# Performance work log

Measured on AMD Instinct MI355X. Metric: run time of the kernel, lower is better.

Reference implementation:

```python
import jax, jax.numpy as jnp
import numpy as np

N_NODES = 100000
N_EDGES = 3200000
N_GRAPHS = 256
HID = 128


def _glorot(key, shape):
    fan_in = shape[1]
    return jax.random.normal(key, shape, dtype=jnp.float32) / jnp.sqrt(jnp.float32(fan_in))


def setup_inputs() -> dict:
    key = jax.random.key(0)
    ks = jax.random.split(key, 16)
    x = jax.random.normal(ks[0], (N_NODES, 50), dtype=jnp.float32)
    edge_index = jax.random.randint(ks[1], (2, N_EDGES), 0, N_NODES, dtype=jnp.int32)
    batch = jnp.sort(jax.random.randint(ks[2], (N_NODES,), 0, N_GRAPHS, dtype=jnp.int32))
    d1, d2, d3 = HID, HID * 2, HID * 4
    params = {
        'w1l': _glorot(ks[3], (d1, 50)), 'b1': jnp.zeros((d1,), jnp.float32), 'w1r': _glorot(ks[4], (d1, 50)),
        'w2l': _glorot(ks[5], (d2, d1)), 'b2': jnp.zeros((d2,), jnp.float32), 'w2r': _glorot(ks[6], (d2, d1)),
        'w3l': _glorot(ks[7], (d3, d2)), 'b3': jnp.zeros((d3,), jnp.float32), 'w3r': _glorot(ks[8], (d3, d2)),
        'fc1_w': _glorot(ks[9], (d2, d3)), 'fc1_b': jnp.zeros((d2,), jnp.float32),
        'fc2_w': _glorot(ks[10], (d1, d2)), 'fc2_b': jnp.zeros((d1,), jnp.float32),
        'cls_w': _glorot(ks[11], (15, d1)), 'cls_b': jnp.zeros((15,), jnp.float32),
    }
    return {'x': x, 'edge_index': edge_index, 'batch': batch, **params}


def _sage_conv(x, src, dst, wl, b, wr):
    # PyG SAGEConv (mean aggr): out = lin_l(mean_j x_j) + lin_r(x_i)
    agg = jax.ops.segment_sum(x[src], dst, num_segments=N_NODES)
    deg = jax.ops.segment_sum(jnp.ones((src.shape[0],), x.dtype), dst, num_segments=N_NODES)
    agg = agg / jnp.maximum(deg, 1.0)[:, None]
    return agg @ wl.T + b + x @ wr.T


def reference(x, edge_index, batch,
              w1l, b1, w1r, w2l, b2, w2r, w3l, b3, w3r,
              fc1_w, fc1_b, fc2_w, fc2_b, cls_w, cls_b):
    src, dst = edge_index[0], edge_index[1]
    # eval mode: dropout is identity
    h = jax.nn.leaky_relu(_sage_conv(x, src, dst, w1l, b1, w1r), negative_slope=0.01)
    h = jax.nn.relu(_sage_conv(h, src, dst, w2l, b2, w2r))
    h = jax.nn.relu(_sage_conv(h, src, dst, w3l, b3, w3r))
    # global mean pool over graphs
    pooled = jax.ops.segment_sum(h, batch, num_segments=N_GRAPHS)
    cnt = jax.ops.segment_sum(jnp.ones((h.shape[0],), h.dtype), batch, num_segments=N_GRAPHS)
    pooled = pooled / jnp.maximum(cnt, 1.0)[:, None]
    z = jax.nn.relu(pooled @ fc1_w.T + fc1_b)
    z = jax.nn.relu(z @ fc2_w.T + fc2_b)
    return z @ cls_w.T + cls_b
```

## Files before the change

kernel.cpp:

```cpp
#include <hip/hip_runtime.h>
#include <hip/hip_bf16.h>

#define N_NODES 100000
#define N_EDGES 3200000
#define N_GRAPHS 256
#define CAP 80
#define NB 1563
#define NPB 64
#define PBLK 512
#define EPB 6250

typedef __hip_bfloat16 bf16;
using f32x4  = __attribute__((ext_vector_type(4))) float;
using f32x2  = __attribute__((ext_vector_type(2))) float;
using short8 = __attribute__((ext_vector_type(8))) short;

__global__ __launch_bounds__(256) void p1_count(const int* __restrict__ dst,
                                                int* __restrict__ bcount) {
    __shared__ int hist[NB];
    int i = blockIdx.x;
    for (int b = threadIdx.x; b < NB; b += 256) hist[b] = 0;
    __syncthreads();
    int base = i * EPB;
    for (int j = threadIdx.x; j < EPB; j += 256)
        atomicAdd(&hist[dst[base + j] >> 6], 1);
    __syncthreads();
    for (int b = threadIdx.x; b < NB; b += 256) bcount[(size_t)b * PBLK + i] = hist[b];
}

__global__ __launch_bounds__(512) void p2a_total(const int* __restrict__ bcount,
                                                 int* __restrict__ btotal) {
    __shared__ int red[512];
    int b = blockIdx.x;
    red[threadIdx.x] = bcount[(size_t)b * PBLK + threadIdx.x];
    __syncthreads();
    for (int off = 256; off > 0; off >>= 1) {
        if (threadIdx.x < off) red[threadIdx.x] += red[threadIdx.x + off];
        __syncthreads();
    }
    if (threadIdx.x == 0) btotal[b] = red[0];
}

__global__ __launch_bounds__(1024) void p2b_scan(const int* __restrict__ btotal,
                                                 int* __restrict__ bbase) {
    __shared__ int buf[1024];
    __shared__ int carry;
    if (threadIdx.x == 0) carry = 0;
    __syncthreads();
    for (int t = 0; t < NB; t += 1024) {
        int i = t + threadIdx.x;
        int v = (i < NB) ? btotal[i] : 0;
        buf[threadIdx.x] = v;
        __syncthreads();
        for (int off = 1; off < 1024; off <<= 1) {
            int tv = (threadIdx.x >= off) ? buf[threadIdx.x - off] : 0;
            __syncthreads();
            buf[threadIdx.x] += tv;
            __syncthreads();
        }
        if (i < NB) bbase[i] = carry + buf[threadIdx.x] - v;
        __syncthreads();
        if (threadIdx.x == 0) carry += buf[1023];
        __syncthreads();
    }
    if (threadIdx.x == 0) bbase[NB] = carry;
}

__global__ __launch_bounds__(512) void p2c_off(const int* __restrict__ bcount,
                                               const int* __restrict__ bbase,
                                               int* __restrict__ off) {
    __shared__ int buf[512];
    int b = blockIdx.x;
    int v = bcount[(size_t)b * PBLK + threadIdx.x];
    buf[threadIdx.x] = v;
    __syncthreads();
    for (int o = 1; o < 512; o <<= 1) {
        int t = (threadIdx.x >= o) ? buf[threadIdx.x - o] : 0;
        __syncthreads();
        buf[threadIdx.x] += t;
        __syncthreads();
    }
    off[(size_t)threadIdx.x * NB + b] = bbase[b] + buf[threadIdx.x] - v;
}

__global__ __launch_bounds__(256) void p3_scatter(const int* __restrict__ src,
                                                  const int* __restrict__ dst,
                                                  const int* __restrict__ off,
                                                  unsigned int* __restrict__ ebuf) {
    __shared__ int loff[NB];
    int i = blockIdx.x;
    for (int b = threadIdx.x; b < NB; b += 256) loff[b] = off[(size_t)i * NB + b];
    __syncthreads();
    int base = i * EPB;
    for (int j = threadIdx.x; j < EPB; j += 256) {
        int d = dst[base + j];
        int p = atomicAdd(&loff[d >> 6], 1);
        ebuf[p] = ((unsigned)src[base + j] << 6) | (unsigned)(d & 63);
    }
}

__global__ __launch_bounds__(256) void p4_csr(const unsigned int* __restrict__ ebuf,
                                              const int* __restrict__ bbase,
                                              int* __restrict__ cols, int* __restrict__ cnt,
                                              float* __restrict__ invdeg) {
    __shared__ int lcnt[NPB];
    int b = blockIdx.x;
    if (threadIdx.x < NPB) lcnt[threadIdx.x] = 0;
    __syncthreads();
    int s = bbase[b], e = bbase[b + 1];
    int n0 = b * NPB;
    for (int j = s + threadIdx.x; j < e; j += 256) {
        unsigned int p = ebuf[j];
        int dl = p & 63;
        int r = atomicAdd(&lcnt[dl], 1);
        if (r < CAP) cols[(size_t)(n0 + dl) * CAP + r] = (int)(p >> 6);
    }
    __syncthreads();
    if (threadIdx.x < NPB) {
        int n = n0 + threadIdx.x;
        if (n < N_NODES) {
            int c = lcnt[threadIdx.x];
            cnt[n] = c;
            invdeg[n] = 1.0f / fmaxf((float)c, 1.0f);
        }
    }
}

__global__ void xprep_kernel(const float* __restrict__ x, bf16* __restrict__ xb,
                             unsigned char* __restrict__ xb8) {
    int t = blockIdx.x * blockDim.x + threadIdx.x;
    if (t >= N_NODES * 64) return;
    int n = t >> 6, f = t & 63;
    float v = (f < 50) ? x[(size_t)n * 50 + f] : 0.f;
    xb[t] = __float2bfloat16(v);
    int p = __builtin_amdgcn_cvt_pk_fp8_f32(v, v, 0, false);
    xb8[t] = (unsigned char)(p & 0xff);
}

__device__ __forceinline__ void wcvt(const float* __restrict__ s, bf16* __restrict__ d,
                                     int Din, int Kp, int lt) {
    int o = lt / Kp, kk = lt % Kp;
    d[lt] = __float2bfloat16(kk < Din ? s[(size_t)o * Din + kk] : 0.f);
}

__global__ void wprep_all_kernel(const float* w1l, const float* w1r,
                                 const float* w2l, const float* w2r,
                                 const float* w3l, const float* w3r,
                                 bf16* w1l_b, bf16* w1r_b, bf16* w2l_b, bf16* w2r_b,
                                 bf16* w3l_b, bf16* w3r_b) {
    int t = blockIdx.x * blockDim.x + threadIdx.x;
    if      (t < 8192)   wcvt(w1l, w1l_b, 50, 64, t);
    else if (t < 16384)  wcvt(w1r, w1r_b, 50, 64, t - 8192);
    else if (t < 49152)  wcvt(w2l, w2l_b, 128, 128, t - 16384);
    else if (t < 81920)  wcvt(w2r, w2r_b, 128, 128, t - 49152);
    else if (t < 212992) wcvt(w3l, w3l_b, 256, 256, t - 81920);
    else if (t < 344064) wcvt(w3r, w3r_b, 256, 256, t - 212992);
}

template <int D>
__global__ void aggv8_kernel(const unsigned char* __restrict__ h8,
                             const int* __restrict__ cnt,
                             const int* __restrict__ cols, const float* __restrict__ invdeg,
                             bf16* __restrict__ AG) {
    constexpr int L = D / 8;
    int n = blockIdx.x * (256 / L) + threadIdx.x / L;
    int lane = threadIdx.x % L;
    if (n >= N_NODES) return;
    const int* cp = cols + (size_t)n * CAP;
    int deg = min(cnt[n], CAP);
    float acc[8] = {};
    auto accum = [&](uint2 v) {
        f32x2 a0 = __builtin_amdgcn_cvt_pk_f32_fp8(v.x, false);
        f32x2 a1 = __builtin_amdgcn_cvt_pk_f32_fp8(v.x, true);
        f32x2 a2 = __builtin_amdgcn_cvt_pk_f32_fp8(v.y, false);
        f32x2 a3 = __builtin_amdgcn_cvt_pk_f32_fp8(v.y, true);
        acc[0] += a0[0]; acc[1] += a0[1]; acc[2] += a1[0]; acc[3] += a1[1];
        acc[4] += a2[0]; acc[5] += a2[1]; acc[6] += a3[0]; acc[7] += a3[1];
    };
    int j = 0;
    for (; j + 8 <= deg; j += 8) {
        uint2 v[8];
#pragma unroll
        for (int q = 0; q < 8; ++q)
            v[q] = *(const uint2*)&h8[(size_t)cp[j + q] * D + lane * 8];
#pragma unroll
        for (int q = 0; q < 8; ++q) accum(v[q]);
    }
    for (; j < deg; ++j) accum(*(const uint2*)&h8[(size_t)cp[j] * D + lane * 8]);
    float inv = invdeg[n];
    union { uint4 u; bf16 hb[8]; } o;
#pragma unroll
    for (int i = 0; i < 8; ++i) o.hb[i] = __float2bfloat16(acc[i] * inv);
    *(uint4*)&AG[(size_t)n * D + lane * 8] = o.u;
}

template <int ACT, int POOL, int OUT8, int NX>
__global__ __launch_bounds__(256) void glds_gemm(
        const bf16* __restrict__ A1, const bf16* __restrict__ A2, int Kh,
        const bf16* __restrict__ B1, const bf16* __restrict__ B2,
        const float* __restrict__ bias, bf16* __restrict__ out,
        unsigned char* __restrict__ out8,
        int M, int Dout,
        const int* __restrict__ batch, float* __restrict__ pooled) {
    __shared__ alignas(16) bf16 As[2][128][32];
    __shared__ alignas(16) bf16 Bs[2][128][32];
    __shared__ int sbatch[128];

    const int gid = blockIdx.x;
    const int group = gid / (8 * NX);
    const int rem = gid % (8 * NX);
    const int xcol = rem >> 3;
    const int ytile = group * 8 + (rem & 7);
    const int MBt = (M + 127) >> 7;
    if (ytile >= MBt) return;

    const int tid = threadIdx.x;
    const int n0 = ytile * 128;
    const int o0 = xcol * 128;

    if (POOL && tid < 128) {
        int n = n0 + tid;
        sbatch[tid] = (n < M) ? batch[n] : -1;
    }

    const int lane = tid & 63;
    const int w = tid >> 6;
    const int wr = w >> 1, wc = w & 1;
    const int lr = lane & 15, hi = lane >> 4;
    const int l4 = lane >> 2;
    const int kc8 = (lane & 3) * 8;

    f32x4 acc[4][4] = {};

    auto stage = [&](int buf, int k0) {
        const bf16* Ap;
        const bf16* Bp;
        int kk;
        if (k0 < Kh) { Ap = A1; Bp = B1; kk = k0; }
        else         { Ap = A2; Bp = B2; kk = k0 - Kh; }
#pragma unroll
        for (int c = 0; c < 2; ++c) {
            int rl = w * 32 + c * 16 + l4;
            size_t ga = (size_t)min(n0 + rl, M - 1) * (size_t)Kh + kk + kc8;
            __builtin_amdgcn_global_load_lds(
                (const __attribute__((address_space(1))) void*)(Ap + ga),
                (__attribute__((address_space(3))) void*)&As[buf][w * 32 + c * 16][0], 16, 0, 0);
            size_t gb = (size_t)(o0 + rl) * (size_t)Kh + kk + kc8;
            __builtin_amdgcn_global_load_lds(
                (const __attribute__((address_space(1))) void*)(Bp + gb),
                (__attribute__((address_space(3))) void*)&Bs[buf][w * 32 + c * 16][0], 16, 0, 0);
        }
    };

    const int nt = (2 * Kh) / 32;
    stage(0, 0);
    asm volatile("s_waitcnt vmcnt(0)\n\ts_barrier" ::: "memory");

    int cur = 0;
    for (int t = 0; t < nt; ++t) {
        if (t + 1 < nt) stage(cur ^ 1, (t + 1) * 32);

        short8 af[4], bfr[4];
#pragma unroll
        for (int m = 0; m < 4; ++m)
            af[m] = *(const short8*)&As[cur][wr * 64 + m * 16 + lr][hi * 8];
#pragma unroll
        for (int n = 0; n < 4; ++n)
            bfr[n] = *(const short8*)&Bs[cur][wc * 64 + n * 16 + lr][hi * 8];
#pragma unroll
        for (int m = 0; m < 4; ++m)
#pragma unroll
            for (int n = 0; n < 4; ++n)
                acc[m][n] = __builtin_amdgcn_mfma_f32_16x16x32_bf16(af[m], bfr[n], acc[m][n], 0, 0, 0);

        if (t + 1 < nt)
            asm volatile("s_waitcnt vmcnt(0)\n\ts_barrier" ::: "memory");
        cur ^= 1;
    }

    float bias_v[4];
#pragma unroll
    for (int n = 0; n < 4; ++n) bias_v[n] = bias[o0 + wc * 64 + n * 16 + lr];

    if (!POOL) {
#pragma unroll
        for (int m = 0; m < 4; ++m) {
#pragma unroll
            for (int j = 0; j < 4; ++j) {
                int row = n0 + wr * 64 + m * 16 + hi * 4 + j;
                if (row < M) {
#pragma unroll
                    for (int n = 0; n < 4; ++n) {
                        int col = o0 + wc * 64 + n * 16 + lr;
                        float s = acc[m][n][j] + bias_v[n];
                        if (ACT == 0) s = (s >= 0.f) ? s : 0.01f * s;
                        else          s = fmaxf(s, 0.f);
                        out[(size_t)row * Dout + col] = __float2bfloat16(s);
                        if (OUT8) {
                            int p = __builtin_amdgcn_cvt_pk_fp8_f32(s, s, 0, false);
                            out8[(size_t)row * Dout + col] = (unsigned char)(p & 0xff);
                        }
                    }
                }
            }
        }
    } else {
        int lastv = min(127, M - 1 - n0);
        int gmin = sbatch[0], gmax = sbatch[lastv];
        for (int g = gmin; g <= gmax; ++g) {
            float s[4] = {0.f, 0.f, 0.f, 0.f};
#pragma unroll
            for (int m = 0; m < 4; ++m) {
#pragma unroll
                for (int j = 0; j < 4; ++j) {
                    int rl = wr * 64 + m * 16 + hi * 4 + j;
                    if (sbatch[rl] == g) {
#pragma unroll
                        for (int n = 0; n < 4; ++n)
                            s[n] += fmaxf(acc[m][n][j] + bias_v[n], 0.f);
                    }
                }
            }
#pragma unroll
            for (int n = 0; n < 4; ++n) {
                float v = s[n];
                v += __shfl_xor(v, 16, 64);
                v += __shfl_xor(v, 32, 64);
                if (hi == 0)
                    atomicAdd(&pooled[(size_t)g * 512 + o0 + wc * 64 + n * 16 + lr], v);
            }
        }
    }
}

__global__ void bounds_kernel(const int* __restrict__ batch, int* __restrict__ gstart) {
    int g = blockIdx.x * blockDim.x + threadIdx.x;
    if (g > N_GRAPHS) return;
    int lo = 0, hi = N_NODES;
    while (lo < hi) {
        int mid = (lo + hi) >> 1;
        if (batch[mid] < g) lo = mid + 1;
        else hi = mid;
    }
    gstart[g] = lo;
}

__global__ void pool_finalize(float* __restrict__ pooled, const int* __restrict__ gstart) {
    int g = blockIdx.x;
    int f = threadIdx.x;
    float cnt = fmaxf((float)(gstart[g + 1] - gstart[g]), 1.0f);
    pooled[(size_t)g * 512 + f] /= cnt;
}

template <int ACT>
__global__ void mlp_kernel(const float* __restrict__ in, const float* __restrict__ w,
                           const float* __restrict__ b, float* __restrict__ out,
                           int M, int K, int O) {
    int t = blockIdx.x * blockDim.x + threadIdx.x;
    if (t >= M * O) return;
    int m = t / O, o = t % O;
    const float* ip = in + (size_t)m * K;
    const float* wp = w + (size_t)o * K;
    float s = 0.f;
    for (int k = 0; k < K; ++k) s += ip[k] * wp[k];
    s += b[o];
    if (ACT) s = fmaxf(s, 0.f);
    out[(size_t)m * O + o] = s;
}

extern "C" void kernel_launch(void* const* d_in, const int* in_sizes, int n_in,
                              void* d_out, int out_size, void* d_ws, size_t ws_size,
                              hipStream_t stream) {
    const float* x     = (const float*)d_in[0];
    const int*   ei    = (const int*)d_in[1];
    const int*   batch = (const int*)d_in[2];
    const float* w1l = (const float*)d_in[3];
    const float* b1  = (const float*)d_in[4];
    const float* w1r = (const float*)d_in[5];
    const float* w2l = (const float*)d_in[6];
    const float* b2  = (const float*)d_in[7];
    const float* w2r = (const float*)d_in[8];
    const float* w3l = (const float*)d_in[9];
    const float* b3  = (const float*)d_in[10];
    const float* w3r = (const float*)d_in[11];
    const float* fc1_w = (const float*)d_in[12];
    const float* fc1_b = (const float*)d_in[13];
    const float* fc2_w = (const float*)d_in[14];
    const float* fc2_b = (const float*)d_in[15];
    const float* cls_w = (const float*)d_in[16];
    const float* cls_b = (const float*)d_in[17];
    float* out = (float*)d_out;

    const int* src = ei;
    const int* dst = ei + N_EDGES;

    char* wsp = (char*)d_ws;
    size_t used = 0;
    auto alloc = [&](size_t bytes) {
        char* p = wsp + used;
        used += (bytes + 255) & ~(size_t)255;
        return p;
    };
    int*   cnt    = (int*)alloc((size_t)N_NODES * 4);
    int*   cols   = (int*)alloc((size_t)N_NODES * CAP * 4);
    float* invdeg = (float*)alloc((size_t)N_NODES * 4);
    int*   gstart = (int*)alloc((size_t)(N_GRAPHS + 1) * 4);
    bf16*  xb     = (bf16*)alloc((size_t)N_NODES * 64 * 2);
    char*  R      = alloc((size_t)N_NODES * 256 * 2);
    bf16*  AG     = (bf16*)R;
    bf16*  h1     = (bf16*)(R + (size_t)N_NODES * 128 * 2);
    bf16*  h2     = (bf16*)alloc((size_t)N_NODES * 256 * 2);
    unsigned char* h1_8 = (unsigned char*)alloc((size_t)N_NODES * 128);
    unsigned char* h2_8 = (unsigned char*)alloc((size_t)N_NODES * 256);
    bf16*  w1l_b  = (bf16*)alloc(128 * 64 * 2);
    bf16*  w1r_b  = (bf16*)alloc(128 * 64 * 2);
    bf16*  w2l_b  = (bf16*)alloc(256 * 128 * 2);
    bf16*  w2r_b  = (bf16*)alloc(256 * 128 * 2);
    bf16*  w3l_b  = (bf16*)alloc(512 * 256 * 2);
    bf16*  w3r_b  = (bf16*)alloc(512 * 256 * 2);
    float* pooled = (float*)alloc((size_t)N_GRAPHS * 512 * 4);
    float* z1     = (float*)alloc((size_t)N_GRAPHS * 256 * 4);
    float* z2     = (float*)alloc((size_t)N_GRAPHS * 128 * 4);

    int* bcount = (int*)h1_8;
    int* btotal = bcount + (size_t)NB * PBLK;
    int* bbase  = btotal + NB;
    int* off    = bbase + NB + 1;
    unsigned int* ebuf = (unsigned int*)h2;
    unsigned char* xb8 = (unsigned char*)h2;

    if (ws_size < used) return;

    p1_count<<<PBLK, 256, 0, stream>>>(dst, bcount);
    p2a_total<<<NB, 512, 0, stream>>>(bcount, btotal);
    p2b_scan<<<1, 1024, 0, stream>>>(btotal, bbase);
    p2c_off<<<NB, 512, 0, stream>>>(bcount, bbase, off);
    p3_scatter<<<PBLK, 256, 0, stream>>>(src, dst, off, ebuf);
    p4_csr<<<NB, 256, 0, stream>>>(ebuf, bbase, cols, cnt, invdeg);
    bounds_kernel<<<2, 160, 0, stream>>>(batch, gstart);

    xprep_kernel<<<(N_NODES * 64 + 255) / 256, 256, 0, stream>>>(x, xb, xb8);
    wprep_all_kernel<<<(344064 + 255) / 256, 256, 0, stream>>>(
        w1l, w1r, w2l, w2r, w3l, w3r, w1l_b, w1r_b, w2l_b, w2r_b, w3l_b, w3r_b);

    const int GB = 98 * 8;

    aggv8_kernel<64><<<(N_NODES * 8 + 255) / 256, 256, 0, stream>>>(
        xb8, cnt, cols, invdeg, AG);
    glds_gemm<0, 0, 1, 1><<<GB, 256, 0, stream>>>(
        AG, xb, 64, w1l_b, w1r_b, b1, h1, h1_8, N_NODES, 128, nullptr, nullptr);

    aggv8_kernel<128><<<(N_NODES * 16 + 255) / 256, 256, 0, stream>>>(
        h1_8, cnt, cols, invdeg, AG);
    glds_gemm<1, 0, 1, 2><<<GB * 2, 256, 0, stream>>>(
        AG, h1, 128, w2l_b, w2r_b, b2, h2, h2_8, N_NODES, 256, nullptr, nullptr);

    aggv8_kernel<256><<<(N_NODES * 32 + 255) / 256, 256, 0, stream>>>(
        h2_8, cnt, cols, invdeg, AG);
    hipMemsetAsync(pooled, 0, (size_t)N_GRAPHS * 512 * 4, stream);
    glds_gemm<1, 1, 0, 4><<<GB * 4, 256, 0, stream>>>(
        AG, h2, 256, w3l_b, w3r_b, b3, nullptr, nullptr, N_NODES, 512, batch, pooled);
    pool_finalize<<<N_GRAPHS, 512, 0, stream>>>(pooled, gstart);

    mlp_kernel<1><<<(N_GRAPHS * 256 + 255) / 256, 256, 0, stream>>>(
        pooled, fc1_w, fc1_b, z1, N_GRAPHS, 512, 256);
    mlp_kernel<1><<<(N_GRAPHS * 128 + 255) / 256, 256, 0, stream>>>(
        z1, fc2_w, fc2_b, z2, N_GRAPHS, 256, 128);
    mlp_kernel<0><<<(N_GRAPHS * 15 + 255) / 256, 256, 0, stream>>>(
        z2, cls_w, cls_b, out, N_GRAPHS, 128, 15);
}
```

Before: 585.4 us.

## Store GEMM A operands and aggregates in fp8, convert to bf16 in-kernel

The aggregation kernel now writes its mean-aggregated features as fp8 instead of bf16, and the layer GEMMs read both A halves (aggregate and self features) from fp8 buffers. The fp8 bytes are converted to bf16 in registers before being written to shared memory, replacing the direct global-to-LDS loads for A. Layer outputs are written only in fp8, and the bf16 copies of x and the hidden layers are no longer produced. This roughly halves A-side and output memory traffic. The cost is extra conversion ALU work, a register-staged A path, and lower precision in the root and aggregate terms.

```diff
diff --git a/kernel.cpp b/kernel.cpp
--- a/kernel.cpp
+++ b/kernel.cpp
@@ -126,13 +126,11 @@
     }
 }
 
-__global__ void xprep_kernel(const float* __restrict__ x, bf16* __restrict__ xb,
-                             unsigned char* __restrict__ xb8) {
+__global__ void xprep_kernel(const float* __restrict__ x, unsigned char* __restrict__ xb8) {
     int t = blockIdx.x * blockDim.x + threadIdx.x;
     if (t >= N_NODES * 64) return;
     int n = t >> 6, f = t & 63;
     float v = (f < 50) ? x[(size_t)n * 50 + f] : 0.f;
-    xb[t] = __float2bfloat16(v);
     int p = __builtin_amdgcn_cvt_pk_fp8_f32(v, v, 0, false);
     xb8[t] = (unsigned char)(p & 0xff);
 }
@@ -161,7 +159,7 @@
 __global__ void aggv8_kernel(const unsigned char* __restrict__ h8,
                              const int* __restrict__ cnt,
                              const int* __restrict__ cols, const float* __restrict__ invdeg,
-                             bf16* __restrict__ AG) {
+                             unsigned char* __restrict__ AG8) {
     constexpr int L = D / 8;
     int n = blockIdx.x * (256 / L) + threadIdx.x / L;
     int lane = threadIdx.x % L;
@@ -188,18 +186,33 @@
     }
     for (; j < deg; ++j) accum(*(const uint2*)&h8[(size_t)cp[j] * D + lane * 8]);
     float inv = invdeg[n];
-    union { uint4 u; bf16 hb[8]; } o;
-#pragma unroll
-    for (int i = 0; i < 8; ++i) o.hb[i] = __float2bfloat16(acc[i] * inv);
-    *(uint4*)&AG[(size_t)n * D + lane * 8] = o.u;
-}
-
-template <int ACT, int POOL, int OUT8, int NX>
-__global__ __launch_bounds__(256) void glds_gemm(
-        const bf16* __restrict__ A1, const bf16* __restrict__ A2, int Kh,
+    uint2 o;
+    int w0 = __builtin_amdgcn_cvt_pk_fp8_f32(acc[0] * inv, acc[1] * inv, 0, false);
+    w0     = __builtin_amdgcn_cvt_pk_fp8_f32(acc[2] * inv, acc[3] * inv, w0, true);
+    int w1 = __builtin_amdgcn_cvt_pk_fp8_f32(acc[4] * inv, acc[5] * inv, 0, false);
+    w1     = __builtin_amdgcn_cvt_pk_fp8_f32(acc[6] * inv, acc[7] * inv, w1, true);
+    o.x = (unsigned)w0; o.y = (unsigned)w1;
+    *(uint2*)&AG8[(size_t)n * D + lane * 8] = o;
+}
+
+__device__ __forceinline__ short8 cvt8(uint2 v) {
+    f32x2 p0 = __builtin_amdgcn_cvt_pk_f32_fp8(v.x, false);
+    f32x2 p1 = __builtin_amdgcn_cvt_pk_f32_fp8(v.x, true);
+    f32x2 p2 = __builtin_amdgcn_cvt_pk_f32_fp8(v.y, false);
+    f32x2 p3 = __builtin_amdgcn_cvt_pk_f32_fp8(v.y, true);
+    union { short8 s; bf16 h[8]; } r;
+    r.h[0] = __float2bfloat16(p0[0]); r.h[1] = __float2bfloat16(p0[1]);
+    r.h[2] = __float2bfloat16(p1[0]); r.h[3] = __float2bfloat16(p1[1]);
+    r.h[4] = __float2bfloat16(p2[0]); r.h[5] = __float2bfloat16(p2[1]);
+    r.h[6] = __float2bfloat16(p3[0]); r.h[7] = __float2bfloat16(p3[1]);
+    return r.s;
+}
+
+template <int ACT, int POOL, int NX>
+__global__ __launch_bounds__(256) void fp8a_gemm(
+        const unsigned char* __restrict__ A1, const unsigned char* __restrict__ A2, int Kh,
         const bf16* __restrict__ B1, const bf16* __restrict__ B2,
-        const float* __restrict__ bias, bf16* __restrict__ out,
-        unsigned char* __restrict__ out8,
+        const float* __restrict__ bias, unsigned char* __restrict__ out8,
         int M, int Dout,
         const int* __restrict__ batch, float* __restrict__ pooled) {
     __shared__ alignas(16) bf16 As[2][128][32];
@@ -232,33 +245,46 @@
 
     f32x4 acc[4][4] = {};
 
-    auto stage = [&](int buf, int k0) {
-        const bf16* Ap;
-        const bf16* Bp;
-        int kk;
-        if (k0 < Kh) { Ap = A1; Bp = B1; kk = k0; }
-        else         { Ap = A2; Bp = B2; kk = k0 - Kh; }
+    const int rl0 = w * 32 + l4;
+    const int rl1 = rl0 + 16;
+
+    auto issueA = [&](int k0, uint2& a0, uint2& a1v) {
+        const unsigned char* Ap = (k0 < Kh) ? A1 : A2;
+        int kk = (k0 < Kh) ? k0 : k0 - Kh;
+        a0  = *(const uint2*)&Ap[(size_t)min(n0 + rl0, M - 1) * Kh + kk + kc8];
+        a1v = *(const uint2*)&Ap[(size_t)min(n0 + rl1, M - 1) * Kh + kk + kc8];
+    };
+    auto issueB = [&](int buf, int k0) {
+        const bf16* Bp = (k0 < Kh) ? B1 : B2;
+        int kk = (k0 < Kh) ? k0 : k0 - Kh;
 #pragma unroll
         for (int c = 0; c < 2; ++c) {
             int rl = w * 32 + c * 16 + l4;
-            size_t ga = (size_t)min(n0 + rl, M - 1) * (size_t)Kh + kk + kc8;
-            __builtin_amdgcn_global_load_lds(
-                (const __attribute__((address_space(1))) void*)(Ap + ga),
-                (__attribute__((address_space(3))) void*)&As[buf][w * 32 + c * 16][0], 16, 0, 0);
             size_t gb = (size_t)(o0 + rl) * (size_t)Kh + kk + kc8;
             __builtin_amdgcn_global_load_lds(
                 (const __attribute__((address_space(1))) void*)(Bp + gb),
                 (__attribute__((address_space(3))) void*)&Bs[buf][w * 32 + c * 16][0], 16, 0, 0);
         }
     };
+    auto writeA = [&](int buf, uint2 a0, uint2 a1v) {
+        *(short8*)&As[buf][rl0][kc8] = cvt8(a0);
+        *(short8*)&As[buf][rl1][kc8] = cvt8(a1v);
+    };
 
     const int nt = (2 * Kh) / 32;
-    stage(0, 0);
-    asm volatile("s_waitcnt vmcnt(0)\n\ts_barrier" ::: "memory");
+    uint2 ra0, ra1;
+    issueA(0, ra0, ra1);
+    issueB(0, 0);
+    asm volatile("s_waitcnt vmcnt(0)" ::: "memory");
+    writeA(0, ra0, ra1);
+    __syncthreads();
 
     int cur = 0;
     for (int t = 0; t < nt; ++t) {
-        if (t + 1 < nt) stage(cur ^ 1, (t + 1) * 32);
+        if (t + 1 < nt) {
+            issueA((t + 1) * 32, ra0, ra1);
+            issueB(cur ^ 1, (t + 1) * 32);
+        }
 
         short8 af[4], bfr[4];
 #pragma unroll
@@ -273,8 +299,11 @@
             for (int n = 0; n < 4; ++n)
                 acc[m][n] = __builtin_amdgcn_mfma_f32_16x16x32_bf16(af[m], bfr[n], acc[m][n], 0, 0, 0);
 
-        if (t + 1 < nt)
-            asm volatile("s_waitcnt vmcnt(0)\n\ts_barrier" ::: "memory");
+        if (t + 1 < nt) {
+            asm volatile("s_waitcnt vmcnt(0)" ::: "memory");
+            writeA(cur ^ 1, ra0, ra1);
+            __syncthreads();
+        }
         cur ^= 1;
     }
 
@@ -295,11 +324,8 @@
                         float s = acc[m][n][j] + bias_v[n];
                         if (ACT == 0) s = (s >= 0.f) ? s : 0.01f * s;
                         else          s = fmaxf(s, 0.f);
-                        out[(size_t)row * Dout + col] = __float2bfloat16(s);
-                        if (OUT8) {
-                            int p = __builtin_amdgcn_cvt_pk_fp8_f32(s, s, 0, false);
-                            out8[(size_t)row * Dout + col] = (unsigned char)(p & 0xff);
-                        }
+                        int p = __builtin_amdgcn_cvt_pk_fp8_f32(s, s, 0, false);
+                        out8[(size_t)row * Dout + col] = (unsigned char)(p & 0xff);
                     }
                 }
             }
@@ -405,11 +431,10 @@
     int*   cols   = (int*)alloc((size_t)N_NODES * CAP * 4);
     float* invdeg = (float*)alloc((size_t)N_NODES * 4);
     int*   gstart = (int*)alloc((size_t)(N_GRAPHS + 1) * 4);
-    bf16*  xb     = (bf16*)alloc((size_t)N_NODES * 64 * 2);
+    char*  xbdead = alloc((size_t)N_NODES * 64 * 2);
     char*  R      = alloc((size_t)N_NODES * 256 * 2);
-    bf16*  AG     = (bf16*)R;
-    bf16*  h1     = (bf16*)(R + (size_t)N_NODES * 128 * 2);
-    bf16*  h2     = (bf16*)alloc((size_t)N_NODES * 256 * 2);
+    unsigned char* AG8 = (unsigned char*)R;
+    char*  S51    = alloc((size_t)N_NODES * 256 * 2);
     unsigned char* h1_8 = (unsigned char*)alloc((size_t)N_NODES * 128);
     unsigned char* h2_8 = (unsigned char*)alloc((size_t)N_NODES * 256);
     bf16*  w1l_b  = (bf16*)alloc(128 * 64 * 2);
@@ -421,13 +446,14 @@
     float* pooled = (float*)alloc((size_t)N_GRAPHS * 512 * 4);
     float* z1     = (float*)alloc((size_t)N_GRAPHS * 256 * 4);
     float* z2     = (float*)alloc((size_t)N_GRAPHS * 128 * 4);
-
-    int* bcount = (int*)h1_8;
+    (void)xbdead;
+
+    int* bcount = (int*)(S51 + 16 * 1024 * 1024);
     int* btotal = bcount + (size_t)NB * PBLK;
     int* bbase  = btotal + NB;
     int* off    = bbase + NB + 1;
-    unsigned int* ebuf = (unsigned int*)h2;
-    unsigned char* xb8 = (unsigned char*)h2;
+    unsigned int* ebuf = (unsigned int*)S51;
+    unsigned char* xb8 = (unsigned char*)S51;
 
     if (ws_size < used) return;
 
@@ -439,27 +465,27 @@
     p4_csr<<<NB, 256, 0, stream>>>(ebuf, bbase, cols, cnt, invdeg);
     bounds_kernel<<<2, 160, 0, stream>>>(batch, gstart);
 
-    xprep_kernel<<<(N_NODES * 64 + 255) / 256, 256, 0, stream>>>(x, xb, xb8);
+    xprep_kernel<<<(N_NODES * 64 + 255) / 256, 256, 0, stream>>>(x, xb8);
     wprep_all_kernel<<<(344064 + 255) / 256, 256, 0, stream>>>(
         w1l, w1r, w2l, w2r, w3l, w3r, w1l_b, w1r_b, w2l_b, w2r_b, w3l_b, w3r_b);
 
     const int GB = 98 * 8;
 
     aggv8_kernel<64><<<(N_NODES * 8 + 255) / 256, 256, 0, stream>>>(
-        xb8, cnt, cols, invdeg, AG);
-    glds_gemm<0, 0, 1, 1><<<GB, 256, 0, stream>>>(
-        AG, xb, 64, w1l_b, w1r_b, b1, h1, h1_8, N_NODES, 128, nullptr, nullptr);
+        xb8, cnt, cols, invdeg, AG8);
+    fp8a_gemm<0, 0, 1><<<GB, 256, 0, stream>>>(
+        AG8, xb8, 64, w1l_b, w1r_b, b1, h1_8, N_NODES, 128, nullptr, nullptr);
 
     aggv8_kernel<128><<<(N_NODES * 16 + 255) / 256, 256, 0, stream>>>(
-        h1_8, cnt, cols, invdeg, AG);
-    glds_gemm<1, 0, 1, 2><<<GB * 2, 256, 0, stream>>>(
-        AG, h1, 128, w2l_b, w2r_b, b2, h2, h2_8, N_NODES, 256, nullptr, nullptr);
+        h1_8, cnt, cols, invdeg, AG8);
+    fp8a_gemm<1, 0, 2><<<GB * 2, 256, 0, stream>>>(
+        AG8, h1_8, 128, w2l_b, w2r_b, b2, h2_8, N_NODES, 256, nullptr, nullptr);
 
     aggv8_kernel<256><<<(N_NODES * 32 + 255) / 256, 256, 0, stream>>>(
-        h2_8, cnt, cols, invdeg, AG);
+        h2_8, cnt, cols, invdeg, AG8);
     hipMemsetAsync(pooled, 0, (size_t)N_GRAPHS * 512 * 4, stream);
-    glds_gemm<1, 1, 0, 4><<<GB * 4, 256, 0, stream>>>(
-        AG, h2, 256, w3l_b, w3r_b, b3, nullptr, nullptr, N_NODES, 512, batch, pooled);
+    fp8a_gemm<1, 1, 4><<<GB * 4, 256, 0, stream>>>(
+        AG8, h2_8, 256, w3l_b, w3r_b, b3, nullptr, N_NODES, 512, batch, pooled);
     pool_finalize<<<N_GRAPHS, 512, 0, stream>>>(pooled, gstart);
 
     mlp_kernel<1><<<(N_GRAPHS * 256 + 255) / 256, 256, 0, stream>>>(
```

Result: faster. 570.5 us (-2.5%).
